# Kernel tuning notes

Measured on AMD Instinct MI355X. Metric: run time of the kernel, lower is better.

The kernel has to match this reference:

```python
import jax, jax.numpy as jnp
import numpy as np

B, IMG, P, S, D, H, HD = 64, 224, 16, 197, 768, 12, 64
MLP, L, PRUNE_AFTER, NCLS = 3072, 12, 4, 1000
N_KEEP = max(1, int(S * 0.5))  # FIXED_RATIO = 0.5 -> 98 kept tokens (plus forced CLS)


def _ln(x, w, b, eps=1e-6):
    m = x.mean(-1, keepdims=True)
    v = ((x - m) ** 2).mean(-1, keepdims=True)
    return (x - m) * jax.lax.rsqrt(v + eps) * w + b


def _block(x, ln1_w, ln1_b, qkv_w, qkv_b, proj_w, proj_b,
           ln2_w, ln2_b, fc1_w, fc1_b, fc2_w, fc2_b, key_mask=None):
    b, s, _ = x.shape
    qkv = _ln(x, ln1_w, ln1_b) @ qkv_w.T + qkv_b           # [B,S,3D]
    qkv = qkv.reshape(b, s, 3, H, HD)
    q, k, v = qkv[:, :, 0], qkv[:, :, 1], qkv[:, :, 2]     # [B,S,H,HD]
    logits = jnp.einsum('bqhd,bkhd->bhqk', q * (HD ** -0.5), k)
    if key_mask is not None:
        # masking pruned keys == varlen attention restricted to kept tokens
        logits = jnp.where(key_mask[:, None, None, :], logits, -1e9)
    attn = jax.nn.softmax(logits, axis=-1)
    out = jnp.einsum('bhqk,bkhd->bqhd', attn, v).reshape(b, s, D)
    x = x + out @ proj_w.T + proj_b
    h = _ln(x, ln2_w, ln2_b)
    h = jax.nn.gelu(h @ fc1_w.T + fc1_b, approximate=False) @ fc2_w.T + fc2_b
    return x + h


def _forward(images, patch_w, patch_b, cls_token, pos_embed,
             ln1_w, ln1_b, qkv_w, qkv_b, proj_w, proj_b,
             ln2_w, ln2_b, fc1_w, fc1_b, fc2_w, fc2_b,
             norm_w, norm_b, head_w, head_b):
    # patch embed: conv stride P == non-overlapping patch projection
    x = jax.lax.conv_general_dilated(images, patch_w, (P, P), 'VALID',
                                     dimension_numbers=('NCHW', 'OIHW', 'NCHW'))
    x = x.reshape(x.shape[0], D, -1).transpose(0, 2, 1) + patch_b       # [B,196,D]
    x = jnp.concatenate([jnp.broadcast_to(cls_token, (x.shape[0], 1, D)), x], axis=1)
    x = x + pos_embed                                                    # [B,197,D]
    for i in range(PRUNE_AFTER):
        x = _block(x, ln1_w[i], ln1_b[i], qkv_w[i], qkv_b[i], proj_w[i], proj_b[i],
                   ln2_w[i], ln2_b[i], fc1_w[i], fc1_b[i], fc2_w[i], fc2_b[i])
    # norm-score topk prune (CLS always kept), as in _threshold_prune
    scores = jnp.linalg.norm(x, axis=-1)                                 # [B,S]
    _, idx = jax.lax.top_k(scores, N_KEEP)
    mask = jnp.zeros((x.shape[0], S), bool)
    mask = mask.at[jnp.arange(x.shape[0])[:, None], idx].set(True).at[:, 0].set(True)
    # Padded-mask form of triton_pack_tokens + flash_attn_varlen: pruned tokens
    # are never attended to (masked keys) and their own outputs are unused.
    for i in range(PRUNE_AFTER, L):
        x = _block(x, ln1_w[i], ln1_b[i], qkv_w[i], qkv_b[i], proj_w[i], proj_b[i],
                   ln2_w[i], ln2_b[i], fc1_w[i], fc1_b[i], fc2_w[i], fc2_b[i],
                   key_mask=mask)
    cls = _ln(x[:, 0], norm_w, norm_b)   # packed[cu[:-1]] is always the CLS token
    return cls @ head_w.T + head_b       # [B, NCLS]


def setup_inputs():
    key = jax.random.key(0)
    ks = iter(jax.random.split(key, 32))
    def rn(shape, s=0.02):
        return jax.random.normal(next(ks), shape, jnp.float32) * s
    return {
        'images': jax.random.normal(next(ks), (B, 3, IMG, IMG), jnp.float32),
        'patch_w': rn((D, 3, P, P)), 'patch_b': jnp.zeros((D,), jnp.float32),
        'cls_token': rn((1, 1, D)), 'pos_embed': rn((1, S, D)),
        'ln1_w': jnp.ones((L, D), jnp.float32), 'ln1_b': jnp.zeros((L, D), jnp.float32),
        'qkv_w': rn((L, 3 * D, D)), 'qkv_b': jnp.zeros((L, 3 * D), jnp.float32),
        'proj_w': rn((L, D, D)), 'proj_b': jnp.zeros((L, D), jnp.float32),
        'ln2_w': jnp.ones((L, D), jnp.float32), 'ln2_b': jnp.zeros((L, D), jnp.float32),
        'fc1_w': rn((L, MLP, D)), 'fc1_b': jnp.zeros((L, MLP), jnp.float32),
        'fc2_w': rn((L, D, MLP)), 'fc2_b': jnp.zeros((L, D), jnp.float32),
        'norm_w': jnp.ones((D,), jnp.float32), 'norm_b': jnp.zeros((D,), jnp.float32),
        'head_w': rn((NCLS, D)), 'head_b': jnp.zeros((NCLS,), jnp.float32),
    }


def reference(images, patch_w, patch_b, cls_token, pos_embed,
              ln1_w, ln1_b, qkv_w, qkv_b, proj_w, proj_b,
              ln2_w, ln2_b, fc1_w, fc1_b, fc2_w, fc2_b,
              norm_w, norm_b, head_w, head_b):
    return _forward(images, patch_w, patch_b, cls_token, pos_embed,
                    ln1_w, ln1_b, qkv_w, qkv_b, proj_w, proj_b,
                    ln2_w, ln2_b, fc1_w, fc1_b, fc2_w, fc2_b,
                    norm_w, norm_b, head_w, head_b)
```

## Files before the change

kernel.cpp:

```cpp
#include <hip/hip_runtime.h>
#include <hip/hip_bf16.h>
#include <cstdint>

#define NH 12
#define SQ 197
#define DIM 768
#define HDIM 64
#define BATCH 64
#define MTOK (BATCH*SQ)
#define MLPD 3072
#define NKEEP 98
#define CSLOT 100
#define MCTOK (BATCH*CSLOT)
#define VLDF 224
#define VLDC 128

typedef __attribute__((ext_vector_type(8))) short bf16x8;
typedef __attribute__((ext_vector_type(8))) unsigned short ushort8;
typedef __attribute__((ext_vector_type(4))) float floatx4;

__device__ __forceinline__ unsigned short f2bf(float f) {
  __hip_bfloat16 h = __float2bfloat16(f);
  return reinterpret_cast<unsigned short&>(h);
}

__device__ __forceinline__ float erf_fast(float x) {
  float ax = fabsf(x);
  float t = 1.f / (1.f + 0.3275911f * ax);
  float y = t * (0.254829592f + t * (-0.284496736f + t * (1.421413741f +
            t * (-1.453152027f + t * 1.061405429f))));
  float r = 1.f - y * __expf(-ax * ax);
  return copysignf(r, x);
}

__device__ __forceinline__ void gload16(const unsigned short* g, unsigned short* l) {
  __builtin_amdgcn_global_load_lds(
      (const __attribute__((address_space(1))) void*)g,
      (__attribute__((address_space(3))) void*)l, 16, 0, 0);
}

enum { EPI_PATCH = 0, EPI_QKV = 1, EPI_RESID = 2, EPI_GELU = 3, EPI_HEAD = 4, EPI_QKVC = 5 };

template<int EPI, bool CHK, int NR>
__device__ __forceinline__ void gemm_epilogue(
    floatx4 (&acc)[4][NR], int m0, int n0, int wr, int wc, int l15, int l4,
    const float* __restrict__ bias, int M, int N,
    float* __restrict__ xresid, const float* __restrict__ pos,
    unsigned short* __restrict__ obf, unsigned short* __restrict__ qb,
    unsigned short* __restrict__ kb, unsigned short* __restrict__ vb,
    float* __restrict__ ofp)
{
#pragma unroll
  for (int mr = 0; mr < 4; ++mr) {
#pragma unroll
    for (int nr = 0; nr < NR; ++nr) {
#pragma unroll
      for (int j = 0; j < 4; ++j) {
        int m = m0 + wr + mr * 16 + l4 * 4 + j;
        int n = n0 + wc + nr * 16 + l15;
        if (CHK && (m >= M || n >= N)) continue;
        float val = acc[mr][nr][j] + bias[n];
        if constexpr (EPI == EPI_PATCH) {
          int b = m / 196, p = m - b * 196;
          xresid[(size_t)(b * SQ + 1 + p) * DIM + n] = val + pos[(1 + p) * DIM + n];
        } else if constexpr (EPI == EPI_QKV || EPI == EPI_QKVC) {
          constexpr int SR = (EPI == EPI_QKV) ? SQ : CSLOT;
          constexpr int VL = (EPI == EPI_QKV) ? VLDF : VLDC;
          int part = n / DIM; int within = n - part * DIM;
          int h = within >> 6, hd = within & 63;
          int b = m / SR, s = m - b * SR;
          if (part == 0)      qb[(((size_t)(b * NH + h)) * SR + s) * HDIM + hd] = f2bf(val * 0.125f);
          else if (part == 1) kb[(((size_t)(b * NH + h)) * SR + s) * HDIM + hd] = f2bf(val);
          else                vb[(((size_t)(b * NH + h)) * HDIM + hd) * VL + s] = f2bf(val);
        } else if constexpr (EPI == EPI_RESID) {
          xresid[(size_t)m * DIM + n] += val;
        } else if constexpr (EPI == EPI_GELU) {
          float g = 0.5f * val * (1.f + erf_fast(val * 0.70710678118654752f));
          obf[(size_t)m * MLPD + n] = f2bf(g);
        } else {
          ofp[(size_t)m * 1000 + n] = val;
        }
      }
    }
  }
}

template<int EPI, int BN>
__global__ __launch_bounds__(256)
void gemm_bf(const unsigned short* __restrict__ A, int lda,
             const unsigned short* __restrict__ Wb, int ldw,
             const float* __restrict__ bias,
             int M, int N, int K,
             float* __restrict__ xresid,
             const float* __restrict__ pos,
             unsigned short* __restrict__ obf,
             unsigned short* __restrict__ qb,
             unsigned short* __restrict__ kb,
             unsigned short* __restrict__ vb,
             float* __restrict__ ofp)
{
  constexpr int NR = BN / 32;
  constexpr int NG = (128 + BN) / 8;
  constexpr int PG = NG / 4;
  __shared__ unsigned short As[128 * 64];
  __shared__ unsigned short Bs[BN * 64];
  const int tid = threadIdx.x;
  const int lane = tid & 63;
  const int w = tid >> 6;
  const int wr = (w >> 1) * 64, wc = (w & 1) * (BN / 2);

  const int gx = gridDim.x;
  const int nwg = gx * gridDim.y;
  const int orig = blockIdx.y * gx + blockIdx.x;
  const int q = nwg >> 3, r = nwg & 7;
  const int xcd = orig & 7, o8 = orig >> 3;
  const int wgid = ((xcd < r) ? xcd * (q + 1) : r * (q + 1) + (xcd - r) * q) + o8;
  const int bx = wgid % gx, by = wgid / gx;
  const int m0 = by * 128, n0 = bx * BN;
  const int l15 = lane & 15, l4 = lane >> 4;

  const int sub = lane & 7, rsub = lane >> 3;
  const int scol = ((sub ^ rsub) << 3);
  const unsigned short* gp[PG];
  unsigned short* lp[PG];
#pragma unroll
  for (int j = 0; j < PG; ++j) {
    int t = w * PG + j;
    if (t < 16) {
      int row = t * 8 + rsub;
      int ra = m0 + row; if (ra > M - 1) ra = M - 1;
      gp[j] = A + (size_t)ra * lda + scol;
      lp[j] = &As[t * 512];
    } else {
      int tb = t - 16;
      int row = tb * 8 + rsub;
      int rb = n0 + row; if (rb > N - 1) rb = N - 1;
      gp[j] = Wb + (size_t)rb * ldw + scol;
      lp[j] = &Bs[tb * 512];
    }
  }

  floatx4 acc[4][NR];
#pragma unroll
  for (int i = 0; i < 4; ++i)
#pragma unroll
    for (int j = 0; j < NR; ++j) acc[i][j] = {0.f, 0.f, 0.f, 0.f};

  for (int kt = 0; kt < K; kt += 64) {
#pragma unroll
    for (int j = 0; j < PG; ++j)
      gload16(gp[j] + kt, lp[j]);
    __syncthreads();
#pragma unroll
    for (int kk = 0; kk < 2; ++kk) {
      bf16x8 af[4], bfr[NR];
#pragma unroll
      for (int mr = 0; mr < 4; ++mr) {
        int row = wr + mr * 16 + l15;
        int cs = (kk * 4 + l4) ^ (row & 7);
        af[mr] = *(const bf16x8*)&As[row * 64 + cs * 8];
      }
#pragma unroll
      for (int nr = 0; nr < NR; ++nr) {
        int row = wc + nr * 16 + l15;
        int cs = (kk * 4 + l4) ^ (row & 7);
        bfr[nr] = *(const bf16x8*)&Bs[row * 64 + cs * 8];
      }
#pragma unroll
      for (int mr = 0; mr < 4; ++mr)
#pragma unroll
        for (int nr = 0; nr < NR; ++nr)
          acc[mr][nr] = __builtin_amdgcn_mfma_f32_16x16x32_bf16(af[mr], bfr[nr], acc[mr][nr], 0, 0, 0);
    }
    __syncthreads();
  }
  if (m0 + 128 <= M && n0 + BN <= N)
    gemm_epilogue<EPI, false, NR>(acc, m0, n0, wr, wc, l15, l4, bias, M, N,
                                  xresid, pos, obf, qb, kb, vb, ofp);
  else
    gemm_epilogue<EPI, true, NR>(acc, m0, n0, wr, wc, l15, l4, bias, M, N,
                                 xresid, pos, obf, qb, kb, vb, ofp);
}

template<int EPI>
__global__ __launch_bounds__(256)
void gemm_f32(const unsigned short* __restrict__ A, int lda,
              const float* __restrict__ Wf, int ldw,
              const float* __restrict__ bias,
              int M, int N, int K,
              float* __restrict__ xresid,
              const float* __restrict__ pos,
              unsigned short* __restrict__ obf,
              unsigned short* __restrict__ qb,
              unsigned short* __restrict__ kb,
              unsigned short* __restrict__ vb,
              float* __restrict__ ofp)
{
  __shared__ unsigned short As[128 * 64];
  __shared__ unsigned short Bs[128 * 64];
  const int tid = threadIdx.x;
  const int lane = tid & 63;
  const int w = tid >> 6;
  const int wr = (w >> 1) * 64, wc = (w & 1) * 64;
  const int m0 = blockIdx.y * 128, n0 = blockIdx.x * 128;
  const int l15 = lane & 15, l4 = lane >> 4;

  floatx4 acc[4][4];
#pragma unroll
  for (int i = 0; i < 4; ++i)
#pragma unroll
    for (int j = 0; j < 4; ++j) acc[i][j] = {0.f, 0.f, 0.f, 0.f};

  for (int kt = 0; kt < K; kt += 64) {
#pragma unroll
    for (int i = 0; i < 4; ++i) {
      int g = tid + 256 * i;
      int row = g >> 3, c = g & 7;
      int sw = (c ^ (row & 7)) * 8;
      int ra = m0 + row; if (ra > M - 1) ra = M - 1;
      ushort8 av = *(const ushort8*)(A + (size_t)ra * lda + kt + c * 8);
      *(ushort8*)&As[row * 64 + sw] = av;
      int rb = n0 + row; if (rb > N - 1) rb = N - 1;
      const float* bs = Wf + (size_t)rb * ldw + kt + c * 8;
      float4 f0 = *(const float4*)bs;
      float4 f1 = *(const float4*)(bs + 4);
      ushort8 bv;
      bv[0] = f2bf(f0.x); bv[1] = f2bf(f0.y); bv[2] = f2bf(f0.z); bv[3] = f2bf(f0.w);
      bv[4] = f2bf(f1.x); bv[5] = f2bf(f1.y); bv[6] = f2bf(f1.z); bv[7] = f2bf(f1.w);
      *(ushort8*)&Bs[row * 64 + sw] = bv;
    }
    __syncthreads();
#pragma unroll
    for (int kk = 0; kk < 2; ++kk) {
      bf16x8 af[4], bfr[4];
#pragma unroll
      for (int mr = 0; mr < 4; ++mr) {
        int row = wr + mr * 16 + l15;
        int cs = (kk * 4 + l4) ^ (row & 7);
        af[mr] = *(const bf16x8*)&As[row * 64 + cs * 8];
      }
#pragma unroll
      for (int nr = 0; nr < 4; ++nr) {
        int row = wc + nr * 16 + l15;
        int cs = (kk * 4 + l4) ^ (row & 7);
        bfr[nr] = *(const bf16x8*)&Bs[row * 64 + cs * 8];
      }
#pragma unroll
      for (int mr = 0; mr < 4; ++mr)
#pragma unroll
        for (int nr = 0; nr < 4; ++nr)
          acc[mr][nr] = __builtin_amdgcn_mfma_f32_16x16x32_bf16(af[mr], bfr[nr], acc[mr][nr], 0, 0, 0);
    }
    __syncthreads();
  }
  if (m0 + 128 <= M && n0 + 128 <= N)
    gemm_epilogue<EPI, false, 4>(acc, m0, n0, wr, wc, l15, l4, bias, M, N,
                                 xresid, pos, obf, qb, kb, vb, ofp);
  else
    gemm_epilogue<EPI, true, 4>(acc, m0, n0, wr, wc, l15, l4, bias, M, N,
                                xresid, pos, obf, qb, kb, vb, ofp);
}

__global__ __launch_bounds__(256)
void cvt_kernel(const float* __restrict__ src, unsigned short* __restrict__ dst, int nchunks)
{
  int i = blockIdx.x * 256 + threadIdx.x;
  if (i >= nchunks) return;
  float4 f0 = *(const float4*)(src + (size_t)i * 8);
  float4 f1 = *(const float4*)(src + (size_t)i * 8 + 4);
  ushort8 v;
  v[0] = f2bf(f0.x); v[1] = f2bf(f0.y); v[2] = f2bf(f0.z); v[3] = f2bf(f0.w);
  v[4] = f2bf(f1.x); v[5] = f2bf(f1.y); v[6] = f2bf(f1.z); v[7] = f2bf(f1.w);
  *(ushort8*)(dst + (size_t)i * 8) = v;
}

__global__ __launch_bounds__(256)
void ln_kernel(const float* __restrict__ x, long long row_stride,
               const float* __restrict__ g, const float* __restrict__ b,
               unsigned short* __restrict__ out)
{
  int row = blockIdx.x;
  const float* xr = x + (size_t)row * row_stride;
  int t = threadIdx.x;
  float v0 = xr[t], v1 = xr[t + 256], v2 = xr[t + 512];
  float s = v0 + v1 + v2, sq = v0 * v0 + v1 * v1 + v2 * v2;
  __shared__ float sb[8];
  for (int o = 32; o; o >>= 1) { s += __shfl_down(s, o); sq += __shfl_down(sq, o); }
  if ((t & 63) == 0) { sb[t >> 6] = s; sb[4 + (t >> 6)] = sq; }
  __syncthreads();
  s = sb[0] + sb[1] + sb[2] + sb[3];
  sq = sb[4] + sb[5] + sb[6] + sb[7];
  float mean = s * (1.f / 768.f);
  float var = sq * (1.f / 768.f) - mean * mean;
  float rstd = rsqrtf(var + 1e-6f);
  unsigned short* orow = out + (size_t)row * DIM;
  orow[t]       = f2bf((v0 - mean) * rstd * g[t]       + b[t]);
  orow[t + 256] = f2bf((v1 - mean) * rstd * g[t + 256] + b[t + 256]);
  orow[t + 512] = f2bf((v2 - mean) * rstd * g[t + 512] + b[t + 512]);
}

template<int NT, int SROWS, int VLD, int PSTR, bool CNT>
__global__ __launch_bounds__(256)
void attn_kernel(const unsigned short* __restrict__ qb,
                 const unsigned short* __restrict__ kb,
                 const unsigned short* __restrict__ vb,
                 const int* __restrict__ cnt,
                 unsigned short* __restrict__ outA)
{
  __shared__ unsigned short Ks[NT * 16 * 64];
  __shared__ unsigned short Ps[4][16 * PSTR];
  int bh = blockIdx.x;
  int b = bh / NH, h = bh - b * NH;
  const int tid = threadIdx.x, lane = tid & 63, w = tid >> 6;
  const int l15 = lane & 15, l4 = lane >> 4;
  const unsigned short* kbase = kb + (size_t)bh * SROWS * HDIM;
  const unsigned short* qbase = qb + (size_t)bh * SROWS * HDIM;
  const unsigned short* vbase = vb + (size_t)bh * HDIM * VLD;
  const int limit = CNT ? cnt[b] : SROWS;

  constexpr int KCH = NT * 16 * 8;
  for (int i = 0; i < (KCH + 255) / 256; ++i) {
    int gch = tid + 256 * i;
    if (gch < KCH) {
      int row = gch >> 3, c = gch & 7;
      int rs = row > SROWS - 1 ? SROWS - 1 : row;
      ushort8 kv = *(const ushort8*)(kbase + (size_t)rs * HDIM + c * 8);
      *(ushort8*)&Ks[row * 64 + ((c ^ (row & 7))) * 8] = kv;
    }
  }
  __syncthreads();

  for (int qt = w; qt < NT; qt += 4) {
    int qrow = qt * 16 + l15; if (qrow > SROWS - 1) qrow = SROWS - 1;
    bf16x8 aq0 = *(const bf16x8*)(qbase + (size_t)qrow * HDIM + l4 * 8);
    bf16x8 aq1 = *(const bf16x8*)(qbase + (size_t)qrow * HDIM + 32 + l4 * 8);

    floatx4 lg[NT];
#pragma unroll
    for (int nt = 0; nt < NT; ++nt) {
      lg[nt] = {0.f, 0.f, 0.f, 0.f};
      int row = nt * 16 + l15;
      int cs0 = (l4) ^ (row & 7);
      int cs1 = (4 + l4) ^ (row & 7);
      bf16x8 bk0 = *(const bf16x8*)&Ks[row * 64 + cs0 * 8];
      bf16x8 bk1 = *(const bf16x8*)&Ks[row * 64 + cs1 * 8];
      lg[nt] = __builtin_amdgcn_mfma_f32_16x16x32_bf16(aq0, bk0, lg[nt], 0, 0, 0);
      lg[nt] = __builtin_amdgcn_mfma_f32_16x16x32_bf16(aq1, bk1, lg[nt], 0, 0, 0);
    }
    float mx[4] = {-1e30f, -1e30f, -1e30f, -1e30f};
#pragma unroll
    for (int nt = 0; nt < NT; ++nt) {
      int col = nt * 16 + l15;
      bool valid = col < limit;
#pragma unroll
      for (int j = 0; j < 4; ++j) {
        float v = valid ? lg[nt][j] : -1e9f;
        lg[nt][j] = v;
        mx[j] = fmaxf(mx[j], v);
      }
    }
#pragma unroll
    for (int j = 0; j < 4; ++j)
      for (int o = 1; o < 16; o <<= 1) mx[j] = fmaxf(mx[j], __shfl_xor(mx[j], o));
    float sm[4] = {0.f, 0.f, 0.f, 0.f};
#pragma unroll
    for (int nt = 0; nt < NT; ++nt)
#pragma unroll
      for (int j = 0; j < 4; ++j) {
        float p = __expf(lg[nt][j] - mx[j]);
        lg[nt][j] = p;
        sm[j] += p;
      }
#pragma unroll
    for (int j = 0; j < 4; ++j) {
      for (int o = 1; o < 16; o <<= 1) sm[j] += __shfl_xor(sm[j], o);
      sm[j] = 1.f / sm[j];
    }
    unsigned short* pw = &Ps[w][0];
#pragma unroll
    for (int nt = 0; nt < NT; ++nt) {
      int col = nt * 16 + l15;
#pragma unroll
      for (int j = 0; j < 4; ++j)
        pw[(l4 * 4 + j) * PSTR + col] = f2bf(lg[nt][j]);
    }
#pragma unroll
    for (int j = 0; j < 4; ++j)
      pw[(l4 * 4 + j) * PSTR + NT * 16 + l15] = 0;
    floatx4 oacc[4];
#pragma unroll
    for (int nr = 0; nr < 4; ++nr) oacc[nr] = {0.f, 0.f, 0.f, 0.f};
#pragma unroll
    for (int ks = 0; ks < VLD / 32; ++ks) {
      bf16x8 ap = *(const bf16x8*)&pw[l15 * PSTR + ks * 32 + l4 * 8];
#pragma unroll
      for (int nr = 0; nr < 4; ++nr) {
        bf16x8 bv = *(const bf16x8*)(vbase + (size_t)(nr * 16 + l15) * VLD + ks * 32 + l4 * 8);
        oacc[nr] = __builtin_amdgcn_mfma_f32_16x16x32_bf16(ap, bv, oacc[nr], 0, 0, 0);
      }
    }
#pragma unroll
    for (int nr = 0; nr < 4; ++nr)
#pragma unroll
      for (int j = 0; j < 4; ++j) {
        int qi = qt * 16 + l4 * 4 + j;
        if (qi < SROWS)
          outA[((size_t)(b * SROWS + qi)) * DIM + h * HDIM + nr * 16 + l15] = f2bf(oacc[nr][j] * sm[j]);
      }
  }
}

__global__ __launch_bounds__(256)
void im2col_kernel(const float* __restrict__ images, unsigned short* __restrict__ out)
{
  int idx = blockIdx.x * 256 + threadIdx.x;
  int token = idx / 96;
  int kc = (idx - token * 96) * 8;
  int b = token / 196, p = token - b * 196;
  int py = p / 14, px = p - py * 14;
  int c = kc >> 8, rem = kc & 255;
  int i = rem >> 4, j0 = rem & 15;
  const float* src = images + (((size_t)(b * 3 + c) * 224 + py * 16 + i) * 224 + px * 16 + j0);
  float4 f0 = *(const float4*)src;
  float4 f1 = *(const float4*)(src + 4);
  ushort8 v;
  v[0] = f2bf(f0.x); v[1] = f2bf(f0.y); v[2] = f2bf(f0.z); v[3] = f2bf(f0.w);
  v[4] = f2bf(f1.x); v[5] = f2bf(f1.y); v[6] = f2bf(f1.z); v[7] = f2bf(f1.w);
  *(ushort8*)(out + (size_t)token * DIM + kc) = v;
}

__global__ __launch_bounds__(256)
void clspos_kernel(const float* __restrict__ cls, const float* __restrict__ pos,
                   float* __restrict__ x)
{
  int idx = blockIdx.x * 256 + threadIdx.x;
  int b = idx / DIM, d = idx - b * DIM;
  x[(size_t)(b * SQ) * DIM + d] = cls[d] + pos[d];
}

__global__ __launch_bounds__(256)
void norms_kernel(const float* __restrict__ x, float* __restrict__ norms)
{
  int row = blockIdx.x * 4 + (threadIdx.x >> 6);
  if (row >= MTOK) return;
  int lane = threadIdx.x & 63;
  const float* xr = x + (size_t)row * DIM;
  float acc = 0.f;
  for (int d = lane; d < DIM; d += 64) { float v = xr[d]; acc += v * v; }
  for (int o = 32; o; o >>= 1) acc += __shfl_down(acc, o);
  if (lane == 0) norms[row] = acc;
}

__global__ __launch_bounds__(256)
void topk_select(const float* __restrict__ norms, short* __restrict__ sidx,
                 int* __restrict__ cntg)
{
  int b = blockIdx.x;
  __shared__ float sc[SQ];
  __shared__ unsigned char keep[SQ];
  int tid = threadIdx.x;
  if (tid < SQ) sc[tid] = norms[b * SQ + tid];
  __syncthreads();
  if (tid < SQ) {
    float mine = sc[tid];
    int rank = 0;
    for (int j = 0; j < SQ; ++j) {
      float v = sc[j];
      rank += (v > mine) || (v == mine && j < tid);
    }
    keep[tid] = (rank < NKEEP) || (tid == 0);
  }
  __syncthreads();
  if (tid == 0) {
    short* row = sidx + b * CSLOT;
    int c = 0;
    for (int s = 0; s < SQ; ++s) if (keep[s]) row[c++] = (short)s;
    cntg[b] = c;
    for (int s = c; s < CSLOT; ++s) row[s] = 0;
  }
}

__global__ __launch_bounds__(192)
void gather_kernel(const float* __restrict__ x, const short* __restrict__ sidx,
                   float* __restrict__ xc)
{
  int g = blockIdx.x;
  int b = g / CSLOT;
  int src = sidx[g];
  const float4* sp = (const float4*)(x + ((size_t)(b * SQ + src)) * DIM);
  float4* dp = (float4*)(xc + (size_t)g * DIM);
  dp[threadIdx.x] = sp[threadIdx.x];
}

template<int EPI, int BN>
static inline void launch_gemm(hipStream_t stream, bool usebf,
                               const unsigned short* A, int lda,
                               const float* Wf, const unsigned short* Wb, int ldw,
                               const float* bias, int M, int N, int K,
                               float* xresid, const float* pos,
                               unsigned short* obf, unsigned short* qb,
                               unsigned short* kb, unsigned short* vb, float* ofp)
{
  if (usebf) {
    dim3 grid((N + BN - 1) / BN, (M + 127) / 128);
    gemm_bf<EPI, BN><<<grid, 256, 0, stream>>>(A, lda, Wb, ldw, bias,
        M, N, K, xresid, pos, obf, qb, kb, vb, ofp);
  } else {
    dim3 grid((N + 127) / 128, (M + 127) / 128);
    gemm_f32<EPI><<<grid, 256, 0, stream>>>(A, lda, Wf, ldw, bias,
        M, N, K, xresid, pos, obf, qb, kb, vb, ofp);
  }
}

extern "C" void kernel_launch(void* const* d_in, const int* in_sizes, int n_in,
                              void* d_out, int out_size, void* d_ws, size_t ws_size,
                              hipStream_t stream)
{
  const float* images    = (const float*)d_in[0];
  const float* patch_w   = (const float*)d_in[1];
  const float* patch_b   = (const float*)d_in[2];
  const float* cls_token = (const float*)d_in[3];
  const float* pos_embed = (const float*)d_in[4];
  const float* ln1_w = (const float*)d_in[5];
  const float* ln1_b = (const float*)d_in[6];
  const float* qkv_w = (const float*)d_in[7];
  const float* qkv_b = (const float*)d_in[8];
  const float* proj_w = (const float*)d_in[9];
  const float* proj_b = (const float*)d_in[10];
  const float* ln2_w = (const float*)d_in[11];
  const float* ln2_b = (const float*)d_in[12];
  const float* fc1_w = (const float*)d_in[13];
  const float* fc1_b = (const float*)d_in[14];
  const float* fc2_w = (const float*)d_in[15];
  const float* fc2_b = (const float*)d_in[16];
  const float* norm_w = (const float*)d_in[17];
  const float* norm_b = (const float*)d_in[18];
  const float* head_w = (const float*)d_in[19];
  const float* head_b = (const float*)d_in[20];

  char* ws = (char*)d_ws;
  size_t off = 0;
  auto alloc = [&](size_t bytes) { void* p = ws + off; off += (bytes + 255) & ~(size_t)255; return p; };
  float* x            = (float*)alloc((size_t)MTOK * DIM * 4);
  float* xc           = (float*)alloc((size_t)MCTOK * DIM * 4);
  unsigned short* xn  = (unsigned short*)alloc((size_t)MTOK * DIM * 2);
  size_t h1_bytes = (size_t)MTOK * MLPD * 2;
  unsigned short* h1  = (unsigned short*)alloc(h1_bytes);
  unsigned short* qb  = h1;
  unsigned short* kb  = qb + (size_t)BATCH * NH * SQ * HDIM;
  unsigned short* vb  = kb + (size_t)BATCH * NH * SQ * HDIM;
  size_t vbytes = (size_t)BATCH * NH * HDIM * VLDF * 2;
  unsigned short* lncls = (unsigned short*)alloc((size_t)64 * DIM * 2);
  float* norms = (float*)alloc((size_t)MTOK * 4);
  short* sidx  = (short*)alloc((size_t)MCTOK * 2);
  int* cnt = (int*)alloc(BATCH * 4);
  size_t n_qkvw = (size_t)12 * 2304 * DIM, n_projw = (size_t)12 * DIM * DIM;
  size_t n_fc1w = (size_t)12 * MLPD * DIM, n_fc2w = (size_t)12 * DIM * MLPD;
  size_t n_patw = (size_t)DIM * DIM, n_headw = (size_t)1000 * DIM;
  unsigned short* wqkv = (unsigned short*)alloc(n_qkvw * 2);
  unsigned short* wproj = (unsigned short*)alloc(n_projw * 2);
  unsigned short* wfc1 = (unsigned short*)alloc(n_fc1w * 2);
  unsigned short* wfc2 = (unsigned short*)alloc(n_fc2w * 2);
  unsigned short* wpat = (unsigned short*)alloc(n_patw * 2);
  unsigned short* whead = (unsigned short*)alloc(n_headw * 2);
  const bool usebf = (off <= ws_size);

  hipMemsetAsync(vb, 0, vbytes, stream);

  if (usebf) {
    cvt_kernel<<<(int)((n_qkvw/8 + 255)/256), 256, 0, stream>>>(qkv_w, wqkv, (int)(n_qkvw/8));
    cvt_kernel<<<(int)((n_projw/8 + 255)/256), 256, 0, stream>>>(proj_w, wproj, (int)(n_projw/8));
    cvt_kernel<<<(int)((n_fc1w/8 + 255)/256), 256, 0, stream>>>(fc1_w, wfc1, (int)(n_fc1w/8));
    cvt_kernel<<<(int)((n_fc2w/8 + 255)/256), 256, 0, stream>>>(fc2_w, wfc2, (int)(n_fc2w/8));
    cvt_kernel<<<(int)((n_patw/8 + 255)/256), 256, 0, stream>>>(patch_w, wpat, (int)(n_patw/8));
    cvt_kernel<<<(int)((n_headw/8 + 255)/256), 256, 0, stream>>>(head_w, whead, (int)(n_headw/8));
  }

  im2col_kernel<<<4704, 256, 0, stream>>>(images, h1);
  launch_gemm<EPI_PATCH, 64>(stream, usebf, h1, DIM, patch_w, wpat, DIM,
      patch_b, 12544, DIM, DIM, x, pos_embed, nullptr, nullptr, nullptr, nullptr, nullptr);
  clspos_kernel<<<192, 256, 0, stream>>>(cls_token, pos_embed, x);

  for (int l = 0; l < 4; ++l) {
    ln_kernel<<<MTOK, 256, 0, stream>>>(x, DIM, ln1_w + l * DIM, ln1_b + l * DIM, xn);
    launch_gemm<EPI_QKV, 128>(stream, usebf, xn, DIM,
        qkv_w + (size_t)l * 2304 * DIM, wqkv + (size_t)l * 2304 * DIM, DIM,
        qkv_b + l * 2304, MTOK, 2304, DIM, nullptr, nullptr, nullptr, qb, kb, vb, nullptr);
    attn_kernel<13, SQ, VLDF, 248, false><<<BATCH * NH, 256, 0, stream>>>(qb, kb, vb, nullptr, xn);
    launch_gemm<EPI_RESID, 64>(stream, usebf, xn, DIM,
        proj_w + (size_t)l * DIM * DIM, wproj + (size_t)l * DIM * DIM, DIM,
        proj_b + l * DIM, MTOK, DIM, DIM, x, nullptr, nullptr, nullptr, nullptr, nullptr, nullptr);
    ln_kernel<<<MTOK, 256, 0, stream>>>(x, DIM, ln2_w + l * DIM, ln2_b + l * DIM, xn);
    launch_gemm<EPI_GELU, 128>(stream, usebf, xn, DIM,
        fc1_w + (size_t)l * MLPD * DIM, wfc1 + (size_t)l * MLPD * DIM, DIM,
        fc1_b + l * MLPD, MTOK, MLPD, DIM, nullptr, nullptr, h1, nullptr, nullptr, nullptr, nullptr);
    launch_gemm<EPI_RESID, 64>(stream, usebf, h1, MLPD,
        fc2_w + (size_t)l * DIM * MLPD, wfc2 + (size_t)l * DIM * MLPD, MLPD,
        fc2_b + l * DIM, MTOK, DIM, MLPD, x, nullptr, nullptr, nullptr, nullptr, nullptr, nullptr);
  }

  norms_kernel<<<(MTOK + 3) / 4, 256, 0, stream>>>(x, norms);
  topk_select<<<BATCH, 256, 0, stream>>>(norms, sidx, cnt);
  gather_kernel<<<MCTOK, 192, 0, stream>>>(x, sidx, xc);

  for (int l = 4; l < 12; ++l) {
    ln_kernel<<<MCTOK, 256, 0, stream>>>(xc, DIM, ln1_w + l * DIM, ln1_b + l * DIM, xn);
    launch_gemm<EPI_QKVC, 128>(stream, usebf, xn, DIM,
        qkv_w + (size_t)l * 2304 * DIM, wqkv + (size_t)l * 2304 * DIM, DIM,
        qkv_b + l * 2304, MCTOK, 2304, DIM, nullptr, nullptr, nullptr, qb, kb, vb, nullptr);
    attn_kernel<7, CSLOT, VLDC, 136, true><<<BATCH * NH, 256, 0, stream>>>(qb, kb, vb, cnt, xn);
    launch_gemm<EPI_RESID, 64>(stream, usebf, xn, DIM,
        proj_w + (size_t)l * DIM * DIM, wproj + (size_t)l * DIM * DIM, DIM,
        proj_b + l * DIM, MCTOK, DIM, DIM, xc, nullptr, nullptr, nullptr, nullptr, nullptr, nullptr);
    ln_kernel<<<MCTOK, 256, 0, stream>>>(xc, DIM, ln2_w + l * DIM, ln2_b + l * DIM, xn);
    launch_gemm<EPI_GELU, 128>(stream, usebf, xn, DIM,
        fc1_w + (size_t)l * MLPD * DIM, wfc1 + (size_t)l * MLPD * DIM, DIM,
        fc1_b + l * MLPD, MCTOK, MLPD, DIM, nullptr, nullptr, h1, nullptr, nullptr, nullptr, nullptr);
    launch_gemm<EPI_RESID, 64>(stream, usebf, h1, MLPD,
        fc2_w + (size_t)l * DIM * MLPD, wfc2 + (size_t)l * DIM * MLPD, MLPD,
        fc2_b + l * DIM, MCTOK, DIM, MLPD, xc, nullptr, nullptr, nullptr, nullptr, nullptr, nullptr);
  }

  ln_kernel<<<64, 256, 0, stream>>>(xc, (long long)CSLOT * DIM, norm_w, norm_b, lncls);
  launch_gemm<EPI_HEAD, 64>(stream, usebf, lncls, DIM, head_w, whead, DIM,
      head_b, 64, 1000, DIM, nullptr, nullptr, nullptr, nullptr, nullptr, nullptr, (float*)d_out);
  (void)in_sizes; (void)n_in; (void)out_size;
}
```

Baseline: 3.715 ms.

## Add 256x256 double-buffered bf16 GEMM for QKV and FC1 projections

Adds a new 512-thread GEMM kernel with 256x256 output tiles, double-buffered LDS staging through direct global-to-LDS loads, and an XCD-aware workgroup remapping. The QKV and FC1 GEMMs, which have wide N, now use it in place of the 128-wide tile kernel. The intent is to raise arithmetic intensity per loaded byte and to overlap the next tile's loads with MFMA work. The cost is 128KB of LDS per block and heavy register use, which limits occupancy. The wide tiles also cause tail waste on M=6400 and 12608.

```diff
diff --git a/kernel.cpp b/kernel.cpp
--- a/kernel.cpp
+++ b/kernel.cpp
@@ -41,9 +41,9 @@
 
 enum { EPI_PATCH = 0, EPI_QKV = 1, EPI_RESID = 2, EPI_GELU = 3, EPI_HEAD = 4, EPI_QKVC = 5 };
 
-template<int EPI, bool CHK, int NR>
+template<int EPI, bool CHK, int MR, int NR>
 __device__ __forceinline__ void gemm_epilogue(
-    floatx4 (&acc)[4][NR], int m0, int n0, int wr, int wc, int l15, int l4,
+    floatx4 (&acc)[MR][NR], int m0, int n0, int wr, int wc, int l15, int l4,
     const float* __restrict__ bias, int M, int N,
     float* __restrict__ xresid, const float* __restrict__ pos,
     unsigned short* __restrict__ obf, unsigned short* __restrict__ qb,
@@ -51,7 +51,7 @@
     float* __restrict__ ofp)
 {
 #pragma unroll
-  for (int mr = 0; mr < 4; ++mr) {
+  for (int mr = 0; mr < MR; ++mr) {
 #pragma unroll
     for (int nr = 0; nr < NR; ++nr) {
 #pragma unroll
@@ -85,6 +85,116 @@
   }
 }
 
+template<int EPI>
+__global__ __launch_bounds__(512, 2)
+void gemm_bf256(const unsigned short* __restrict__ A, int lda,
+                const unsigned short* __restrict__ Wb, int ldw,
+                const float* __restrict__ bias,
+                int M, int N, int K,
+                float* __restrict__ xresid,
+                const float* __restrict__ pos,
+                unsigned short* __restrict__ obf,
+                unsigned short* __restrict__ qb,
+                unsigned short* __restrict__ kb,
+                unsigned short* __restrict__ vb,
+                float* __restrict__ ofp)
+{
+  __shared__ unsigned short As[2][256 * 64];
+  __shared__ unsigned short Bs[2][256 * 64];
+  const int tid = threadIdx.x;
+  const int lane = tid & 63;
+  const int w = tid >> 6;
+  const int wr = (w >> 2) * 128;
+  const int wc = (w & 3) * 64;
+
+  const int gx = gridDim.x;
+  const int nwg = gx * gridDim.y;
+  const int orig = blockIdx.y * gx + blockIdx.x;
+  const int q = nwg >> 3, r = nwg & 7;
+  const int xcd = orig & 7, o8 = orig >> 3;
+  const int wgid = ((xcd < r) ? xcd * (q + 1) : r * (q + 1) + (xcd - r) * q) + o8;
+  const int bx = wgid % gx, by = wgid / gx;
+  const int m0 = by * 256, n0 = bx * 256;
+  const int l15 = lane & 15, l4 = lane >> 4;
+
+  const int sub = lane & 7, rsub = lane >> 3;
+  const int scol = ((sub ^ rsub) << 3);
+  const bool isA = (w < 4);
+  const unsigned short* gp[8];
+  int ldst[8];
+#pragma unroll
+  for (int j = 0; j < 8; ++j) {
+    int row = (w & 3) * 64 + j * 8 + rsub;
+    if (isA) {
+      int ra = m0 + row; if (ra > M - 1) ra = M - 1;
+      gp[j] = A + (size_t)ra * lda + scol;
+    } else {
+      int rb = n0 + row; if (rb > N - 1) rb = N - 1;
+      gp[j] = Wb + (size_t)rb * ldw + scol;
+    }
+    ldst[j] = ((w & 3) * 8 + j) * 512;
+  }
+
+  floatx4 acc[8][4];
+#pragma unroll
+  for (int i = 0; i < 8; ++i)
+#pragma unroll
+    for (int j = 0; j < 4; ++j) acc[i][j] = {0.f, 0.f, 0.f, 0.f};
+
+  auto STAGE = [&](int buf, int kt) {
+    unsigned short* base = isA ? &As[buf][0] : &Bs[buf][0];
+#pragma unroll
+    for (int j = 0; j < 8; ++j)
+      gload16(gp[j] + kt, base + ldst[j]);
+  };
+
+  const int nk = K >> 6;
+  STAGE(0, 0);
+  int cur = 0;
+  for (int ki = 0; ki < nk; ++ki) {
+    if (ki + 1 < nk) {
+      STAGE(cur ^ 1, (ki + 1) << 6);
+      asm volatile("s_waitcnt vmcnt(8)" ::: "memory");
+    } else {
+      asm volatile("s_waitcnt vmcnt(0)" ::: "memory");
+    }
+    __builtin_amdgcn_sched_barrier(0);
+    __builtin_amdgcn_s_barrier();
+    const unsigned short* Ac = &As[cur][0];
+    const unsigned short* Bc = &Bs[cur][0];
+#pragma unroll
+    for (int kk = 0; kk < 2; ++kk) {
+      bf16x8 af[8], bfr[4];
+#pragma unroll
+      for (int mr = 0; mr < 8; ++mr) {
+        int row = wr + mr * 16 + l15;
+        int cs = (kk * 4 + l4) ^ (row & 7);
+        af[mr] = *(const bf16x8*)&Ac[row * 64 + cs * 8];
+      }
+#pragma unroll
+      for (int nr = 0; nr < 4; ++nr) {
+        int row = wc + nr * 16 + l15;
+        int cs = (kk * 4 + l4) ^ (row & 7);
+        bfr[nr] = *(const bf16x8*)&Bc[row * 64 + cs * 8];
+      }
+#pragma unroll
+      for (int mr = 0; mr < 8; ++mr)
+#pragma unroll
+        for (int nr = 0; nr < 4; ++nr)
+          acc[mr][nr] = __builtin_amdgcn_mfma_f32_16x16x32_bf16(af[mr], bfr[nr], acc[mr][nr], 0, 0, 0);
+    }
+    __builtin_amdgcn_sched_barrier(0);
+    __builtin_amdgcn_s_barrier();
+    cur ^= 1;
+  }
+  if (m0 + 256 <= M && n0 + 256 <= N)
+    gemm_epilogue<EPI, false, 8, 4>(acc, m0, n0, wr, wc, l15, l4, bias, M, N,
+                                    xresid, pos, obf, qb, kb, vb, ofp);
+  else
+    gemm_epilogue<EPI, true, 8, 4>(acc, m0, n0, wr, wc, l15, l4, bias, M, N,
+                                   xresid, pos, obf, qb, kb, vb, ofp);
+}
+
 template<int EPI, int BN>
 __global__ __launch_bounds__(256)
 void gemm_bf(const unsigned short* __restrict__ A, int lda,
@@ -175,11 +285,11 @@
     __syncthreads();
   }
   if (m0 + 128 <= M && n0 + BN <= N)
-    gemm_epilogue<EPI, false, NR>(acc, m0, n0, wr, wc, l15, l4, bias, M, N,
-                                  xresid, pos, obf, qb, kb, vb, ofp);
+    gemm_epilogue<EPI, false, 4, NR>(acc, m0, n0, wr, wc, l15, l4, bias, M, N,
+                                     xresid, pos, obf, qb, kb, vb, ofp);
   else
-    gemm_epilogue<EPI, true, NR>(acc, m0, n0, wr, wc, l15, l4, bias, M, N,
-                                 xresid, pos, obf, qb, kb, vb, ofp);
+    gemm_epilogue<EPI, true, 4, NR>(acc, m0, n0, wr, wc, l15, l4, bias, M, N,
+                                    xresid, pos, obf, qb, kb, vb, ofp);
 }
 
 template<int EPI>
@@ -254,11 +364,11 @@
     __syncthreads();
   }
   if (m0 + 128 <= M && n0 + 128 <= N)
-    gemm_epilogue<EPI, false, 4>(acc, m0, n0, wr, wc, l15, l4, bias, M, N,
-                                 xresid, pos, obf, qb, kb, vb, ofp);
+    gemm_epilogue<EPI, false, 4, 4>(acc, m0, n0, wr, wc, l15, l4, bias, M, N,
+                                    xresid, pos, obf, qb, kb, vb, ofp);
   else
-    gemm_epilogue<EPI, true, 4>(acc, m0, n0, wr, wc, l15, l4, bias, M, N,
-                                xresid, pos, obf, qb, kb, vb, ofp);
+    gemm_epilogue<EPI, true, 4, 4>(acc, m0, n0, wr, wc, l15, l4, bias, M, N,
+                                   xresid, pos, obf, qb, kb, vb, ofp);
 }
 
 __global__ __launch_bounds__(256)
@@ -509,6 +619,25 @@
     dim3 grid((N + 127) / 128, (M + 127) / 128);
     gemm_f32<EPI><<<grid, 256, 0, stream>>>(A, lda, Wf, ldw, bias,
         M, N, K, xresid, pos, obf, qb, kb, vb, ofp);
+  }
+}
+
+template<int EPI>
+static inline void launch_gemm256(hipStream_t stream, bool usebf,
+                                  const unsigned short* A, int lda,
+                                  const float* Wf, const unsigned short* Wb, int ldw,
+                                  const float* bias, int M, int N, int K,
+                                  unsigned short* obf, unsigned short* qb,
+                                  unsigned short* kb, unsigned short* vb)
+{
+  if (usebf) {
+    dim3 grid(N / 256, (M + 255) / 256);
+    gemm_bf256<EPI><<<grid, 512, 0, stream>>>(A, lda, Wb, ldw, bias,
+        M, N, K, nullptr, nullptr, obf, qb, kb, vb, nullptr);
+  } else {
+    dim3 grid((N + 127) / 128, (M + 127) / 128);
+    gemm_f32<EPI><<<grid, 256, 0, stream>>>(A, lda, Wf, ldw, bias,
+        M, N, K, nullptr, nullptr, obf, qb, kb, vb, nullptr);
   }
 }
 
@@ -583,17 +712,17 @@
 
   for (int l = 0; l < 4; ++l) {
     ln_kernel<<<MTOK, 256, 0, stream>>>(x, DIM, ln1_w + l * DIM, ln1_b + l * DIM, xn);
-    launch_gemm<EPI_QKV, 128>(stream, usebf, xn, DIM,
+    launch_gemm256<EPI_QKV>(stream, usebf, xn, DIM,
         qkv_w + (size_t)l * 2304 * DIM, wqkv + (size_t)l * 2304 * DIM, DIM,
-        qkv_b + l * 2304, MTOK, 2304, DIM, nullptr, nullptr, nullptr, qb, kb, vb, nullptr);
+        qkv_b + l * 2304, MTOK, 2304, DIM, nullptr, qb, kb, vb);
     attn_kernel<13, SQ, VLDF, 248, false><<<BATCH * NH, 256, 0, stream>>>(qb, kb, vb, nullptr, xn);
     launch_gemm<EPI_RESID, 64>(stream, usebf, xn, DIM,
         proj_w + (size_t)l * DIM * DIM, wproj + (size_t)l * DIM * DIM, DIM,
         proj_b + l * DIM, MTOK, DIM, DIM, x, nullptr, nullptr, nullptr, nullptr, nullptr, nullptr);
     ln_kernel<<<MTOK, 256, 0, stream>>>(x, DIM, ln2_w + l * DIM, ln2_b + l * DIM, xn);
-    launch_gemm<EPI_GELU, 128>(stream, usebf, xn, DIM,
+    launch_gemm256<EPI_GELU>(stream, usebf, xn, DIM,
         fc1_w + (size_t)l * MLPD * DIM, wfc1 + (size_t)l * MLPD * DIM, DIM,
-        fc1_b + l * MLPD, MTOK, MLPD, DIM, nullptr, nullptr, h1, nullptr, nullptr, nullptr, nullptr);
+        fc1_b + l * MLPD, MTOK, MLPD, DIM, h1, nullptr, nullptr, nullptr);
     launch_gemm<EPI_RESID, 64>(stream, usebf, h1, MLPD,
         fc2_w + (size_t)l * DIM * MLPD, wfc2 + (size_t)l * DIM * MLPD, MLPD,
         fc2_b + l * DIM, MTOK, DIM, MLPD, x, nullptr, nullptr, nullptr, nullptr, nullptr, nullptr);
@@ -605,17 +734,17 @@
 
   for (int l = 4; l < 12; ++l) {
     ln_kernel<<<MCTOK, 256, 0, stream>>>(xc, DIM, ln1_w + l * DIM, ln1_b + l * DIM, xn);
-    launch_gemm<EPI_QKVC, 128>(stream, usebf, xn, DIM,
+    launch_gemm256<EPI_QKVC>(stream, usebf, xn, DIM,
         qkv_w + (size_t)l * 2304 * DIM, wqkv + (size_t)l * 2304 * DIM, DIM,
-        qkv_b + l * 2304, MCTOK, 2304, DIM, nullptr, nullptr, nullptr, qb, kb, vb, nullptr);
+        qkv_b + l * 2304, MCTOK, 2304, DIM, nullptr, qb, kb, vb);
     attn_kernel<7, CSLOT, VLDC, 136, true><<<BATCH * NH, 256, 0, stream>>>(qb, kb, vb, cnt, xn);
     launch_gemm<EPI_RESID, 64>(stream, usebf, xn, DIM,
         proj_w + (size_t)l * DIM * DIM, wproj + (size_t)l * DIM * DIM, DIM,
         proj_b + l * DIM, MCTOK, DIM, DIM, xc, nullptr, nullptr, nullptr, nullptr, nullptr, nullptr);
     ln_kernel<<<MCTOK, 256, 0, stream>>>(xc, DIM, ln2_w + l * DIM, ln2_b + l * DIM, xn);
-    launch_gemm<EPI_GELU, 128>(stream, usebf, xn, DIM,
+    launch_gemm256<EPI_GELU>(stream, usebf, xn, DIM,
         fc1_w + (size_t)l * MLPD * DIM, wfc1 + (size_t)l * MLPD * DIM, DIM,
-        fc1_b + l * MLPD, MCTOK, MLPD, DIM, nullptr, nullptr, h1, nullptr, nullptr, nullptr, nullptr);
+        fc1_b + l * MLPD, MCTOK, MLPD, DIM, h1, nullptr, nullptr, nullptr);
     launch_gemm<EPI_RESID, 64>(stream, usebf, h1, MLPD,
         fc2_w + (size_t)l * DIM * MLPD, wfc2 + (size_t)l * DIM * MLPD, MLPD,
         fc2_b + l * DIM, MCTOK, DIM, MLPD, xc, nullptr, nullptr, nullptr, nullptr, nullptr, nullptr);
```

Result: no change. 3.771 ms (+1.5%).
